# Kernel tuning notes

Hardware: AMD Instinct MI355X
Metric: run time of the kernel (lower is better)

## Reference

```python
import jax, jax.numpy as jnp
import numpy as np
from jax import lax

INPUT_DIM = 16
H1 = 5
H2 = 50
NUM_CLASSES = 20
B = 4096
T = 512


def _lstm(x, w_ih, w_hh, b_ih, b_hh, hidden):
    # x: [B, T, D]; PyTorch LSTM gate order i, f, g, o; returns all hidden states [B, T, H]
    xg = jnp.einsum('btd,gd->btg', x, w_ih) + (b_ih + b_hh)  # [B, T, 4H]
    xg_t = jnp.swapaxes(xg, 0, 1)  # [T, B, 4H]
    h0 = jnp.zeros((x.shape[0], hidden), x.dtype)
    c0 = jnp.zeros((x.shape[0], hidden), x.dtype)

    def step(carry, xt):
        h, c = carry
        g = xt + h @ w_hh.T  # [B, 4H]
        i, f, gg, o = jnp.split(g, 4, axis=-1)
        i = jax.nn.sigmoid(i)
        f = jax.nn.sigmoid(f)
        gg = jnp.tanh(gg)
        o = jax.nn.sigmoid(o)
        c = f * c + i * gg
        h = o * jnp.tanh(c)
        return (h, c), h

    _, hs = lax.scan(step, (h0, c0), xg_t)
    return jnp.swapaxes(hs, 0, 1)  # [B, T, H]


def setup_inputs() -> dict:
    key = jax.random.key(0)
    ks = jax.random.split(key, 12)
    s1 = 1.0 / np.sqrt(H1)
    s2 = 1.0 / np.sqrt(H2)
    u = lambda k, shape, s: jax.random.uniform(k, shape, jnp.float32, -s, s)
    return {
        'x': jax.random.normal(ks[0], (B, T, INPUT_DIM), jnp.float32),
        'w_ih1': u(ks[1], (4 * H1, INPUT_DIM), s1),
        'w_hh1': u(ks[2], (4 * H1, H1), s1),
        'b_ih1': u(ks[3], (4 * H1,), s1),
        'b_hh1': u(ks[4], (4 * H1,), s1),
        'w_ih2': u(ks[5], (4 * H2, H1), s2),
        'w_hh2': u(ks[6], (4 * H2, H2), s2),
        'b_ih2': u(ks[7], (4 * H2,), s2),
        'b_hh2': u(ks[8], (4 * H2,), s2),
        'fc_w': u(ks[9], (NUM_CLASSES, H2), s2),
        'fc_b': u(ks[10], (NUM_CLASSES,), s2),
    }


def reference(x, w_ih1, w_hh1, b_ih1, b_hh1, w_ih2, w_hh2, b_ih2, b_hh2, fc_w, fc_b):
    h1 = _lstm(x, w_ih1, w_hh1, b_ih1, b_hh1, H1)   # [B, T, 5]
    h2 = _lstm(h1, w_ih2, w_hh2, b_ih2, b_hh2, H2)  # [B, T, 50]
    feat = h2[:, -1, :]  # last timestep; dropout is identity in eval mode
    out = feat @ fc_w.T + fc_b  # [B, num_classes]
    return (out, feat)
```

## Files before the change

### kernel.cpp

```cpp
#include <hip/hip_runtime.h>
#include <stdint.h>

#define B_TOTAL 4096
#define T_STEPS 512
#define IN_DIM 16
#define H1 5
#define H2 50
#define NCLS 20
#define BATCH 8
#define XFS 40

typedef __attribute__((ext_vector_type(8))) short bf16x8;
typedef __attribute__((ext_vector_type(4))) float f32x4;

#define LOG2E 1.44269504f
#define C2L   2.88539008f
#define C2L2  5.77078016f

__device__ inline float rcp1pexp2(float y){
  return __builtin_amdgcn_rcpf(1.0f + __builtin_amdgcn_exp2f(y));
}

__device__ inline unsigned pack_top(float a, float b){
  return __builtin_amdgcn_perm(__float_as_uint(a), __float_as_uint(b), 0x07060302u);
}
__device__ inline void cvt_store(unsigned short* dh, unsigned short* dl, float4 v){
  uint2 H, L;
  H.x = pack_top(v.y, v.x);
  H.y = pack_top(v.w, v.z);
  float r0 = v.x - __uint_as_float(__float_as_uint(v.x) & 0xFFFF0000u);
  float r1 = v.y - __uint_as_float(__float_as_uint(v.y) & 0xFFFF0000u);
  float r2 = v.z - __uint_as_float(__float_as_uint(v.z) & 0xFFFF0000u);
  float r3 = v.w - __uint_as_float(__float_as_uint(v.w) & 0xFFFF0000u);
  L.x = pack_top(r1, r0);
  L.y = pack_top(r3, r2);
  *(uint2*)dh = H; *(uint2*)dl = L;
}
__device__ inline void split1(float h, unsigned short& hi, unsigned short& lo){
  unsigned u = __float_as_uint(h);
  hi = (unsigned short)(u >> 16);
  float r = h - __uint_as_float(u & 0xFFFF0000u);
  lo = (unsigned short)(__float_as_uint(r) >> 16);
}
__device__ inline void wsplit(float w, short& hi, short& lo){
  unsigned u = __float_as_uint(w);
  hi = (short)(u >> 16);
  float r = w - __uint_as_float(u & 0xFFFF0000u);
  lo = (short)(__float_as_uint(r) >> 16);
}
__device__ inline void xsplit(float4 a, float4 b, bf16x8& H, bf16x8& L){
  short h,l;
  wsplit(a.x,h,l); H[0]=h; L[0]=l;
  wsplit(a.y,h,l); H[1]=h; L[1]=l;
  wsplit(a.z,h,l); H[2]=h; L[2]=l;
  wsplit(a.w,h,l); H[3]=h; L[3]=l;
  wsplit(b.x,h,l); H[4]=h; L[4]=l;
  wsplit(b.y,h,l); H[5]=h; L[5]=l;
  wsplit(b.z,h,l); H[6]=h; L[6]=l;
  wsplit(b.w,h,l); H[7]=h; L[7]=l;
}

#define LDS_FENCE() __asm__ volatile("s_waitcnt lgkmcnt(0)" ::: "memory")
#define BARRIER()   __asm__ volatile("s_barrier" ::: "memory")

__global__ __launch_bounds__(256, 2) void lstm_fused_kernel(
    const float* __restrict__ x,
    const float* __restrict__ w_ih1, const float* __restrict__ w_hh1,
    const float* __restrict__ b_ih1, const float* __restrict__ b_hh1,
    const float* __restrict__ w_ih2, const float* __restrict__ w_hh2,
    const float* __restrict__ b_ih2, const float* __restrict__ b_hh2,
    const float* __restrict__ fc_w, const float* __restrict__ fc_b,
    float* __restrict__ out)
{
  const int tid  = threadIdx.x;
  const int lane = tid & 63;
  const int wave = tid >> 6;
  const int l15  = lane & 15;
  const int quad = lane >> 4;
  const int b0   = blockIdx.x * BATCH;

  __shared__ __align__(16) unsigned short a2h[2][16*72], a2l[2][16*72];
  __shared__ __align__(16) unsigned short xfh[2][16*XFS], xfl[2][16*XFS];
  __shared__ float h2f[BATCH*52];

  const bf16x8 zero8 = {0,0,0,0,0,0,0,0};
  const f32x4  zero4 = {0.f,0.f,0.f,0.f};

  bf16x8 Bh[4][3], Bl[4][3];
  f32x4 biasv[4];
  float cst[4] = {0.f,0.f,0.f,0.f};

#pragma unroll
  for (int tt=0; tt<4; ++tt)
#pragma unroll
    for (int kt=0; kt<3; ++kt){ Bh[tt][kt]=zero8; Bl[tt][kt]=zero8; }

  if (wave < 3){
    const int c = wave*16 + l15;
#pragma unroll
    for (int tt=0; tt<4; ++tt){
      const float gsc = (tt == 2) ? C2L : LOG2E;
      const int grow = tt*H2 + c;
#pragma unroll
      for (int kt=0; kt<2; ++kt){
#pragma unroll
        for (int j=0;j<8;j++){
          const int kk = kt*32 + quad*8 + j;
          float w = 0.f;
          if (kk < H2)         w = w_hh2[grow*H2 + kk];
          else if (kk < H2+H1) w = w_ih2[grow*H1 + (kk-H2)];
          w *= gsc;
          short hi, lo; wsplit(w, hi, lo);
          Bh[tt][kt][j] = hi; Bl[tt][kt][j] = lo;
        }
      }
      const float bias = gsc * (b_ih2[grow] + b_hh2[grow]);
      biasv[tt][0]=bias; biasv[tt][1]=bias; biasv[tt][2]=bias; biasv[tt][3]=bias;
    }
  } else {
#pragma unroll
    for (int tt=0; tt<4; ++tt){
      const float gsc = (tt == 2) ? C2L : LOG2E;
      float bias = 0.f;
      if (l15 < 2){
        const int grow = tt*H2 + 48 + l15;
#pragma unroll
        for (int kt=0; kt<2; ++kt){
#pragma unroll
          for (int j=0;j<8;j++){
            const int kk = kt*32 + quad*8 + j;
            float w = 0.f;
            if (kk < H2)         w = w_hh2[grow*H2 + kk];
            else if (kk < H2+H1) w = w_ih2[grow*H1 + (kk-H2)];
            w *= gsc;
            short hi, lo; wsplit(w, hi, lo);
            Bh[tt][kt][j] = hi; Bl[tt][kt][j] = lo;
          }
        }
        bias = gsc * (b_ih2[grow] + b_hh2[grow]);
      } else if (l15 < 7){
        const int e = l15 - 2;
        const int grow = tt*H1 + e;
#pragma unroll
        for (int j=0;j<8;j++){
          const int kk = 32 + quad*8 + j;
          float w1 = (kk >= H2 && kk < H2+H1) ? gsc * w_hh1[grow*H1 + (kk-H2)] : 0.f;
          short hi, lo; wsplit(w1, hi, lo);
          Bh[tt][1][j] = hi; Bl[tt][1][j] = lo;
          const int k2 = quad*8 + j;
          float w2 = (k2 < IN_DIM) ? gsc * w_ih1[grow*IN_DIM + k2] : 0.f;
          wsplit(w2, hi, lo);
          Bh[tt][2][j] = hi; Bl[tt][2][j] = lo;
        }
        bias = gsc * (b_ih1[grow] + b_hh1[grow]);
      }
      biasv[tt][0]=bias; biasv[tt][1]=bias; biasv[tt][2]=bias; biasv[tt][3]=bias;
    }
  }

  { unsigned short* p = &a2h[0][0]; for (int i=tid;i<2*16*72;i+=256)  p[i]=0; }
  { unsigned short* p = &a2l[0][0]; for (int i=tid;i<2*16*72;i+=256)  p[i]=0; }
  { unsigned short* p = &xfh[0][0]; for (int i=tid;i<2*16*XFS;i+=256) p[i]=0; }
  { unsigned short* p = &xfl[0][0]; for (int i=tid;i<2*16*XFS;i+=256) p[i]=0; }
  __syncthreads();

  const bool xprod = (wave == 0) && (lane < 32);
  const int pxb = lane >> 2;
  const int pxd = (lane & 3) * 4;
  const float* pxbase = &x[(size_t)(b0+pxb)*T_STEPS*IN_DIM + pxd];
  float4 PA, PB;
  if (xprod){
    float4 v1 = *(const float4*)(pxbase + 1*IN_DIM);
    cvt_store(&xfh[1][pxb*XFS+pxd], &xfl[1][pxb*XFS+pxd], v1);
    PA = *(const float4*)(pxbase + 2*IN_DIM);
  }

  if (wave == 3){
    bf16x8 XAh = zero8, XAl = zero8;
    if (quad < 2 && l15 < BATCH){
      const float* xp = &x[(size_t)(b0+l15)*T_STEPS*IN_DIM + quad*8];
      xsplit(*(const float4*)xp, *(const float4*)(xp+4), XAh, XAl);
    }
    f32x4 acc[4];
#pragma unroll
    for (int tt=0; tt<4; ++tt){
      f32x4 c2 = __builtin_amdgcn_mfma_f32_16x16x32_bf16(XAh, Bh[tt][2], biasv[tt], 0,0,0);
      c2 = __builtin_amdgcn_mfma_f32_16x16x32_bf16(XAl, Bh[tt][2], c2, 0,0,0);
      c2 = __builtin_amdgcn_mfma_f32_16x16x32_bf16(XAh, Bl[tt][2], c2, 0,0,0);
      acc[tt] = c2;
    }
    const bool isl1 = (l15 >= 2) && (l15 < 7) && (quad < 2);
#pragma unroll
    for (int r=0;r<4;r++){
      float gi = rcp1pexp2(-acc[0][r]);
      float gf = rcp1pexp2(-acc[1][r]);
      float gg = fmaf(-C2L2, rcp1pexp2(acc[2][r]), C2L);
      float go = rcp1pexp2(-acc[3][r]);
      float cn = fmaf(gf, cst[r], gi * gg);
      if (isl1){
        cst[r] = cn;
        float h = go * fmaf(-2.0f, rcp1pexp2(cn), 1.0f);
        unsigned short hh, hl; split1(h, hh, hl);
        const int row = quad*4 + r;
        a2h[0][row*72 + 48 + l15] = hh;
        a2l[0][row*72 + 48 + l15] = hl;
      }
    }
  }
  LDS_FENCE(); BARRIER();

#define ACT_BLOCK(ACC_, HV_) \
    _Pragma("unroll") \
    for (int r=0;r<4;r++){ \
      float gi = rcp1pexp2(-ACC_[0][r]); \
      float gf = rcp1pexp2(-ACC_[1][r]); \
      float gg = fmaf(-C2L2, rcp1pexp2(ACC_[2][r]), C2L);  \
      float go = rcp1pexp2(-ACC_[3][r]); \
      cst[r] = fmaf(gf, cst[r], gi * gg); \
      HV_[r] = go * fmaf(-2.0f, rcp1pexp2(cst[r]), 1.0f); \
    }

#define MAIN_BODY(T_, RD_, WR_, PXW_, PXL_) do { \
    if (xprod){ \
      cvt_store(&xfh[RD_][pxb*XFS+pxd], &xfl[RD_][pxb*XFS+pxd], PXW_);  \
      const int nidx_ = ((T_)+3 < T_STEPS) ? (T_)+3 : T_STEPS-1; \
      PXL_ = *(const float4*)(pxbase + (size_t)nidx_*IN_DIM);           \
    } \
    const int rb_ = l15*72; \
    bf16x8 ah0 = *(const bf16x8*)&a2h[RD_][rb_ +      quad*8]; \
    bf16x8 al0 = *(const bf16x8*)&a2l[RD_][rb_ +      quad*8]; \
    bf16x8 ah1 = *(const bf16x8*)&a2h[RD_][rb_ + 32 + quad*8]; \
    bf16x8 al1 = *(const bf16x8*)&a2l[RD_][rb_ + 32 + quad*8]; \
    f32x4 acc[4]; \
    if (wave < 3){ \
      _Pragma("unroll") \
      for (int tt=0; tt<4; ++tt){ \
        f32x4 c0 = __builtin_amdgcn_mfma_f32_16x16x32_bf16(ah0, Bh[tt][0], biasv[tt], 0,0,0); \
        c0 = __builtin_amdgcn_mfma_f32_16x16x32_bf16(al0, Bh[tt][0], c0, 0,0,0); \
        c0 = __builtin_amdgcn_mfma_f32_16x16x32_bf16(ah0, Bl[tt][0], c0, 0,0,0); \
        f32x4 c1 = __builtin_amdgcn_mfma_f32_16x16x32_bf16(ah1, Bh[tt][1], zero4, 0,0,0); \
        c1 = __builtin_amdgcn_mfma_f32_16x16x32_bf16(al1, Bh[tt][1], c1, 0,0,0); \
        c1 = __builtin_amdgcn_mfma_f32_16x16x32_bf16(ah1, Bl[tt][1], c1, 0,0,0); \
        acc[tt] = c0 + c1; \
      } \
    } else { \
      bf16x8 xfH = *(const bf16x8*)&xfh[WR_][l15*XFS + quad*8]; \
      bf16x8 xfL = *(const bf16x8*)&xfl[WR_][l15*XFS + quad*8]; \
      _Pragma("unroll") \
      for (int tt=0; tt<4; ++tt){ \
        f32x4 c0 = __builtin_amdgcn_mfma_f32_16x16x32_bf16(ah0, Bh[tt][0], biasv[tt], 0,0,0); \
        c0 = __builtin_amdgcn_mfma_f32_16x16x32_bf16(al0, Bh[tt][0], c0, 0,0,0); \
        c0 = __builtin_amdgcn_mfma_f32_16x16x32_bf16(ah0, Bl[tt][0], c0, 0,0,0); \
        f32x4 c1 = __builtin_amdgcn_mfma_f32_16x16x32_bf16(ah1, Bh[tt][1], zero4, 0,0,0); \
        c1 = __builtin_amdgcn_mfma_f32_16x16x32_bf16(al1, Bh[tt][1], c1, 0,0,0); \
        c1 = __builtin_amdgcn_mfma_f32_16x16x32_bf16(ah1, Bl[tt][1], c1, 0,0,0); \
        f32x4 c2 = __builtin_amdgcn_mfma_f32_16x16x32_bf16(xfH, Bh[tt][2], zero4, 0,0,0); \
        c2 = __builtin_amdgcn_mfma_f32_16x16x32_bf16(xfL, Bh[tt][2], c2, 0,0,0); \
        c2 = __builtin_amdgcn_mfma_f32_16x16x32_bf16(xfH, Bl[tt][2], c2, 0,0,0); \
        acc[tt] = (c0 + c1) + c2; \
      } \
    } \
    float hv[4]; \
    ACT_BLOCK(acc, hv) \
    if (wave < 3){ \
      if (quad < 2){ \
        const int wrb = quad*4*72 + wave*16 + l15; \
        _Pragma("unroll") \
        for (int r=0;r<4;r++){ \
          unsigned short hh, hl; split1(hv[r], hh, hl); \
          a2h[WR_][wrb + r*72] = hh; \
          a2l[WR_][wrb + r*72] = hl; \
        } \
        if ((T_) == T_STEPS-1){ \
          _Pragma("unroll") \
          for (int r=0;r<4;r++){ \
            out[(size_t)B_TOTAL*NCLS + (size_t)(b0+quad*4+r)*H2 + wave*16+l15] = hv[r]; \
            h2f[(quad*4+r)*52 + wave*16+l15] = hv[r]; \
          } \
        } \
      } \
    } else if (l15 < 7 && quad < 2){ \
      const int wrb = quad*4*72 + 48 + l15;   \
      _Pragma("unroll") \
      for (int r=0;r<4;r++){ \
        unsigned short hh, hl; split1(hv[r], hh, hl); \
        a2h[WR_][wrb + r*72] = hh; \
        a2l[WR_][wrb + r*72] = hl; \
      } \
      if ((T_) == T_STEPS-1 && l15 < 2){ \
        _Pragma("unroll") \
        for (int r=0;r<4;r++){ \
          out[(size_t)B_TOTAL*NCLS + (size_t)(b0+quad*4+r)*H2 + 48+l15] = hv[r]; \
          h2f[(quad*4+r)*52 + 48+l15] = hv[r]; \
        } \
      } \
    } \
  } while(0)

  for (int t2 = 0; t2 < T_STEPS; t2 += 2){
    MAIN_BODY(t2,   0, 1, PA, PB);
    LDS_FENCE(); BARRIER();
    MAIN_BODY(t2+1, 1, 0, PB, PA);
    LDS_FENCE(); BARRIER();
  }

#undef MAIN_BODY
#undef ACT_BLOCK

  __syncthreads();
  for (int i = tid; i < BATCH*NCLS; i += 256){
    const int b = i / NCLS, o = i % NCLS;
    float s = fc_b[o];
#pragma unroll 10
    for (int k=0;k<H2;k++) s += fc_w[o*H2+k] * h2f[b*52+k];
    out[(size_t)(b0+b)*NCLS + o] = s;
  }
}

extern "C" void kernel_launch(void* const* d_in, const int* in_sizes, int n_in,
                              void* d_out, int out_size, void* d_ws, size_t ws_size,
                              hipStream_t stream) {
  const float* x     = (const float*)d_in[0];
  const float* w_ih1 = (const float*)d_in[1];
  const float* w_hh1 = (const float*)d_in[2];
  const float* b_ih1 = (const float*)d_in[3];
  const float* b_hh1 = (const float*)d_in[4];
  const float* w_ih2 = (const float*)d_in[5];
  const float* w_hh2 = (const float*)d_in[6];
  const float* b_ih2 = (const float*)d_in[7];
  const float* b_hh2 = (const float*)d_in[8];
  const float* fc_w  = (const float*)d_in[9];
  const float* fc_b  = (const float*)d_in[10];
  float* out = (float*)d_out;

  lstm_fused_kernel<<<dim3(B_TOTAL/BATCH), dim3(256), 0, stream>>>(
      x, w_ih1, w_hh1, b_ih1, b_hh1, w_ih2, w_hh2, b_ih2, b_hh2, fc_w, fc_b, out);
}
```

Measured before the change: 727.4 us.

## Fill all 16 MFMA rows with batch elements, halving block count

Each block now handles 16 batch rows instead of 8, so every row of the 16x16 MFMA tiles carries useful work. This halves the grid to 256 blocks, and the launch bound drops to one block per SIMD group. The activation and store code is restructured to run for all quads, and the x prefetch now uses all 64 lanes of wave 0. The trade-off is half as many blocks in flight, which means fewer waves to hide the serial recurrence latency, though a 256-CU device is roughly covered.

```diff
diff --git a/kernel.cpp b/kernel.cpp
--- a/kernel.cpp
+++ b/kernel.cpp
@@ -7,7 +7,6 @@
 #define H1 5
 #define H2 50
 #define NCLS 20
-#define BATCH 8
 #define XFS 40
 
 typedef __attribute__((ext_vector_type(8))) short bf16x8;
@@ -63,7 +62,7 @@
 #define LDS_FENCE() __asm__ volatile("s_waitcnt lgkmcnt(0)" ::: "memory")
 #define BARRIER()   __asm__ volatile("s_barrier" ::: "memory")
 
-__global__ __launch_bounds__(256, 2) void lstm_fused_kernel(
+__global__ __launch_bounds__(256, 1) void lstm_fused_kernel(
     const float* __restrict__ x,
     const float* __restrict__ w_ih1, const float* __restrict__ w_hh1,
     const float* __restrict__ b_ih1, const float* __restrict__ b_hh1,
@@ -77,11 +76,11 @@
   const int wave = tid >> 6;
   const int l15  = lane & 15;
   const int quad = lane >> 4;
-  const int b0   = blockIdx.x * BATCH;
+  const int b0   = blockIdx.x * 16;
 
   __shared__ __align__(16) unsigned short a2h[2][16*72], a2l[2][16*72];
   __shared__ __align__(16) unsigned short xfh[2][16*XFS], xfl[2][16*XFS];
-  __shared__ float h2f[BATCH*52];
+  __shared__ float h2f[16*52];
 
   const bf16x8 zero8 = {0,0,0,0,0,0,0,0};
   const f32x4  zero4 = {0.f,0.f,0.f,0.f};
@@ -164,7 +163,7 @@
   { unsigned short* p = &xfl[0][0]; for (int i=tid;i<2*16*XFS;i+=256) p[i]=0; }
   __syncthreads();
 
-  const bool xprod = (wave == 0) && (lane < 32);
+  const bool xprod = (wave == 0);
   const int pxb = lane >> 2;
   const int pxd = (lane & 3) * 4;
   const float* pxbase = &x[(size_t)(b0+pxb)*T_STEPS*IN_DIM + pxd];
@@ -177,7 +176,7 @@
 
   if (wave == 3){
     bf16x8 XAh = zero8, XAl = zero8;
-    if (quad < 2 && l15 < BATCH){
+    if (quad < 2){
       const float* xp = &x[(size_t)(b0+l15)*T_STEPS*IN_DIM + quad*8];
       xsplit(*(const float4*)xp, *(const float4*)(xp+4), XAh, XAl);
     }
@@ -189,7 +188,7 @@
       c2 = __builtin_amdgcn_mfma_f32_16x16x32_bf16(XAh, Bl[tt][2], c2, 0,0,0);
       acc[tt] = c2;
     }
-    const bool isl1 = (l15 >= 2) && (l15 < 7) && (quad < 2);
+    const bool isl1 = (l15 >= 2) && (l15 < 7);
 #pragma unroll
     for (int r=0;r<4;r++){
       float gi = rcp1pexp2(-acc[0][r]);
@@ -208,17 +207,6 @@
     }
   }
   LDS_FENCE(); BARRIER();
-
-#define ACT_BLOCK(ACC_, HV_) \
-    _Pragma("unroll") \
-    for (int r=0;r<4;r++){ \
-      float gi = rcp1pexp2(-ACC_[0][r]); \
-      float gf = rcp1pexp2(-ACC_[1][r]); \
-      float gg = fmaf(-C2L2, rcp1pexp2(ACC_[2][r]), C2L);  \
-      float go = rcp1pexp2(-ACC_[3][r]); \
-      cst[r] = fmaf(gf, cst[r], gi * gg); \
-      HV_[r] = go * fmaf(-2.0f, rcp1pexp2(cst[r]), 1.0f); \
-    }
 
 #define MAIN_BODY(T_, RD_, WR_, PXW_, PXL_) do { \
     if (xprod){ \
@@ -260,38 +248,44 @@
         acc[tt] = (c0 + c1) + c2; \
       } \
     } \
-    float hv[4]; \
-    ACT_BLOCK(acc, hv) \
+     \
     if (wave < 3){ \
-      if (quad < 2){ \
-        const int wrb = quad*4*72 + wave*16 + l15; \
-        _Pragma("unroll") \
-        for (int r=0;r<4;r++){ \
-          unsigned short hh, hl; split1(hv[r], hh, hl); \
+      const int wrb = quad*4*72 + wave*16 + l15; \
+      _Pragma("unroll") \
+      for (int r=0;r<4;r++){ \
+        float gi = rcp1pexp2(-acc[0][r]); \
+        float gf = rcp1pexp2(-acc[1][r]); \
+        float gg = fmaf(-C2L2, rcp1pexp2(acc[2][r]), C2L); \
+        float go = rcp1pexp2(-acc[3][r]); \
+        cst[r] = fmaf(gf, cst[r], gi * gg); \
+        float h = go * fmaf(-2.0f, rcp1pexp2(cst[r]), 1.0f); \
+        unsigned short hh, hl; split1(h, hh, hl); \
+        a2h[WR_][wrb + r*72] = hh; \
+        a2l[WR_][wrb + r*72] = hl; \
+        if ((T_) == T_STEPS-1){ \
+          out[(size_t)B_TOTAL*NCLS + (size_t)(b0+quad*4+r)*H2 + wave*16+l15] = h; \
+          h2f[(quad*4+r)*52 + wave*16+l15] = h; \
+        } \
+      } \
+    } else { \
+      const int wrb = quad*4*72 + 48 + l15;   \
+      const bool wv_ = l15 < 7; \
+      _Pragma("unroll") \
+      for (int r=0;r<4;r++){ \
+        float gi = rcp1pexp2(-acc[0][r]); \
+        float gf = rcp1pexp2(-acc[1][r]); \
+        float gg = fmaf(-C2L2, rcp1pexp2(acc[2][r]), C2L); \
+        float go = rcp1pexp2(-acc[3][r]); \
+        cst[r] = fmaf(gf, cst[r], gi * gg); \
+        float h = go * fmaf(-2.0f, rcp1pexp2(cst[r]), 1.0f); \
+        if (wv_){ \
+          unsigned short hh, hl; split1(h, hh, hl); \
           a2h[WR_][wrb + r*72] = hh; \
           a2l[WR_][wrb + r*72] = hl; \
-        } \
-        if ((T_) == T_STEPS-1){ \
-          _Pragma("unroll") \
-          for (int r=0;r<4;r++){ \
-            out[(size_t)B_TOTAL*NCLS + (size_t)(b0+quad*4+r)*H2 + wave*16+l15] = hv[r]; \
-            h2f[(quad*4+r)*52 + wave*16+l15] = hv[r]; \
+          if ((T_) == T_STEPS-1 && l15 < 2){ \
+            out[(size_t)B_TOTAL*NCLS + (size_t)(b0+quad*4+r)*H2 + 48+l15] = h; \
+            h2f[(quad*4+r)*52 + 48+l15] = h; \
           } \
-        } \
-      } \
-    } else if (l15 < 7 && quad < 2){ \
-      const int wrb = quad*4*72 + 48 + l15;   \
-      _Pragma("unroll") \
-      for (int r=0;r<4;r++){ \
-        unsigned short hh, hl; split1(hv[r], hh, hl); \
-        a2h[WR_][wrb + r*72] = hh; \
-        a2l[WR_][wrb + r*72] = hl; \
-      } \
-      if ((T_) == T_STEPS-1 && l15 < 2){ \
-        _Pragma("unroll") \
-        for (int r=0;r<4;r++){ \
-          out[(size_t)B_TOTAL*NCLS + (size_t)(b0+quad*4+r)*H2 + 48+l15] = hv[r]; \
-          h2f[(quad*4+r)*52 + 48+l15] = hv[r]; \
         } \
       } \
     } \
@@ -305,10 +299,9 @@
   }
 
 #undef MAIN_BODY
-#undef ACT_BLOCK
 
   __syncthreads();
-  for (int i = tid; i < BATCH*NCLS; i += 256){
+  for (int i = tid; i < 16*NCLS; i += 256){
     const int b = i / NCLS, o = i % NCLS;
     float s = fc_b[o];
 #pragma unroll 10
@@ -333,6 +326,6 @@
   const float* fc_b  = (const float*)d_in[10];
   float* out = (float*)d_out;
 
-  lstm_fused_kernel<<<dim3(B_TOTAL/BATCH), dim3(256), 0, stream>>>(
+  lstm_fused_kernel<<<dim3(B_TOTAL/16), dim3(256), 0, stream>>>(
       x, w_ih1, w_hh1, b_ih1, b_hh1, w_ih2, w_hh2, b_ih2, b_hh2, fc_w, fc_b, out);
 }
```

After: 614.6 us. 15.5% less time.
